# Kernel optimization log

Hardware: AMD Instinct MI355X
Metric: run time of the kernel (lower is better)

## Reference

```python
import jax, jax.numpy as jnp
import numpy as np

N0, N1, N2 = 500000, 100000, 20000
E1, E2 = 1600000, 320000
DIN, DH, DOUT = 128, 256, 128
EPS_BN = 1e-5
EPS_NORM = 1e-12


def setup_inputs() -> dict:
    key = jax.random.key(0)
    k = jax.random.split(key, 16)
    s = 0.05
    return {
        "x": jax.random.normal(k[0], (N0, DIN), jnp.float32),
        "src1": jax.random.randint(k[1], (E1,), 0, N0),
        "dst1": jax.random.randint(k[2], (E1,), 0, N1),
        "src2": jax.random.randint(k[3], (E2,), 0, N1),
        "dst2": jax.random.randint(k[4], (E2,), 0, N2),
        "n1": N1,
        "n2": N2,
        "W1_1": jax.random.normal(k[5], (DH, DIN), jnp.float32) * s,
        "W2_1": jax.random.normal(k[6], (DH, DIN), jnp.float32) * s,
        "b2_1": jax.random.normal(k[7], (DH,), jnp.float32) * s,
        "gamma1": jax.random.uniform(k[8], (DH,), jnp.float32, 0.5, 1.5),
        "beta1": jax.random.normal(k[9], (DH,), jnp.float32) * s,
        "mean1": jax.random.normal(k[10], (DH,), jnp.float32) * s,
        "var1": jax.random.uniform(k[11], (DH,), jnp.float32, 0.5, 1.5),
        "W1_2": jax.random.normal(k[12], (DOUT, DH), jnp.float32) * s,
        "W2_2": jax.random.normal(k[13], (DOUT, DH), jnp.float32) * s,
        "b2_2": jax.random.normal(k[14], (DOUT,), jnp.float32) * s,
    }


def _mean_agg(h, src, dst, n_target):
    # torch_sparse.matmul(adj_t, h, reduce='mean'): per-target mean of neighbor rows
    ssum = jax.ops.segment_sum(h[src], dst, num_segments=n_target)
    cnt = jax.ops.segment_sum(jnp.ones(src.shape, h.dtype), dst, num_segments=n_target)
    return ssum / jnp.maximum(cnt, 1.0)[:, None]


def _l2norm(h):
    # F.normalize(h, p=2, dim=1)
    n = jnp.sqrt(jnp.sum(h * h, axis=1, keepdims=True))
    return h / jnp.maximum(n, EPS_NORM)


def reference(x, src1, dst1, src2, dst2, n1, n2,
              W1_1, W2_1, b2_1, gamma1, beta1, mean1, var1,
              W1_2, W2_2, b2_2):
    # --- layer 1: SageConv(in=128, out=256) ---
    h_n = _mean_agg(x, src1, dst1, n1)                 # [n1, DIN]
    h = x[:n1] @ W1_1.T + (h_n @ W2_1.T + b2_1)        # [n1, DH]
    h = _l2norm(h)
    # BatchNorm1d (eval mode: running stats), then ReLU; dropout is identity in eval
    h = gamma1 * (h - mean1) * jax.lax.rsqrt(var1 + EPS_BN) + beta1
    h = jax.nn.relu(h)
    # --- layer 2: SageConv(in=256, out=128) ---
    h_n2 = _mean_agg(h, src2, dst2, n2)                # [n2, DH]
    out = h[:n2] @ W1_2.T + (h_n2 @ W2_2.T + b2_2)     # [n2, DOUT]
    return _l2norm(out)
```

## Files before the change

### kernel.cpp

```cpp
#include <hip/hip_runtime.h>
#include <hip/hip_bf16.h>

#define N1C  100000
#define N2C  20000
#define DIN_ 128
#define DH_  256
#define DOUT_ 128
#define CAP_LOG2 6
#define CAP_     64

#define BIN_SHIFT 7
#define NBIN1 782
#define NBIN2 157
#define NBINS 939
#define CAP_BIN 3072
#define CHUNK_A 8192

typedef unsigned short ushort_t;
typedef unsigned int   uint_t;
typedef __attribute__((ext_vector_type(8))) short bf16x8;
typedef __attribute__((ext_vector_type(4))) float f32x4;

__device__ __forceinline__ float bf2f(ushort_t u) {
    return __uint_as_float(((uint_t)u) << 16);
}
__device__ __forceinline__ ushort_t f2bf(float f) {
    uint_t x = __float_as_uint(f);
    x += 0x7fffu + ((x >> 16) & 1u);
    return (ushort_t)(x >> 16);
}

__global__ __launch_bounds__(256) void convert_all_kernel(
    const float* __restrict__ src, ushort_t* __restrict__ dst, long long n8,
    const float* __restrict__ w0, const float* __restrict__ w1,
    const float* __restrict__ w2, const float* __restrict__ w3,
    ushort_t* __restrict__ wdst)
{
    const long long t = (long long)blockIdx.x * 256 + threadIdx.x;
    if (t < n8) {
        const float4 v0 = *(const float4*)(src + t * 8);
        const float4 v1 = *(const float4*)(src + t * 8 + 4);
        uint4 o;
        o.x = (uint_t)f2bf(v0.x) | ((uint_t)f2bf(v0.y) << 16);
        o.y = (uint_t)f2bf(v0.z) | ((uint_t)f2bf(v0.w) << 16);
        o.z = (uint_t)f2bf(v1.x) | ((uint_t)f2bf(v1.y) << 16);
        o.w = (uint_t)f2bf(v1.z) | ((uint_t)f2bf(v1.w) << 16);
        *(uint4*)(dst + t * 8) = o;
    } else {
        const long long t2 = t - n8;
        if (t2 >= 16384) return;
        const int mat = (int)(t2 >> 12);
        const long long idx = (long long)(t2 & 4095) * 8;
        const float* s = (mat == 0) ? w0 : (mat == 1) ? w1 : (mat == 2) ? w2 : w3;
        const float4 v0 = *(const float4*)(s + idx);
        const float4 v1 = *(const float4*)(s + idx + 4);
        uint4 o;
        o.x = (uint_t)f2bf(v0.x) | ((uint_t)f2bf(v0.y) << 16);
        o.y = (uint_t)f2bf(v0.z) | ((uint_t)f2bf(v0.w) << 16);
        o.z = (uint_t)f2bf(v1.x) | ((uint_t)f2bf(v1.y) << 16);
        o.w = (uint_t)f2bf(v1.z) | ((uint_t)f2bf(v1.w) << 16);
        *(uint4*)(wdst + (long long)mat * 32768 + idx) = o;
    }
}

__global__ __launch_bounds__(256) void bin_edges_kernel(
    const int* __restrict__ src1, const int* __restrict__ dst1, int E1,
    const int* __restrict__ src2, const int* __restrict__ dst2, int E2,
    int* __restrict__ gTail, uint2* __restrict__ binBuf)
{
    __shared__ int hist[NBINS];
    __shared__ int binOff[NBINS];
    __shared__ int runc[NBINS];
    __shared__ int gb[NBINS];
    __shared__ uint2 stage[CHUNK_A];
    __shared__ int wtot[4];

    const int tid = threadIdx.x;
    const int tE = E1 + E2;
    const int c0 = blockIdx.x * CHUNK_A;
    const int cend = (c0 + CHUNK_A < tE) ? (c0 + CHUNK_A) : tE;
    const int ccnt = cend - c0;

    for (int b = tid; b < NBINS; b += 256) hist[b] = 0;
    __syncthreads();

    for (int i = c0 + tid; i < cend; i += 256) {
        int d, bin;
        if (i < E1) { d = dst1[i];      bin = d >> BIN_SHIFT; }
        else        { d = dst2[i - E1]; bin = NBIN1 + (d >> BIN_SHIFT); }
        atomicAdd(&hist[bin], 1);
    }
    __syncthreads();

    {
        int h[4]; int tsum = 0;
        #pragma unroll
        for (int k = 0; k < 4; ++k) {
            const int b = tid * 4 + k;
            h[k] = (b < NBINS) ? hist[b] : 0;
            tsum += h[k];
        }
        int s = tsum;
        #pragma unroll
        for (int o = 1; o < 64; o <<= 1) {
            int t = __shfl_up(s, (unsigned)o);
            if ((tid & 63) >= o) s += t;
        }
        if ((tid & 63) == 63) wtot[tid >> 6] = s;
        __syncthreads();
        int wpre = 0;
        #pragma unroll
        for (int k = 0; k < 4; ++k) wpre += (k < (tid >> 6)) ? wtot[k] : 0;
        int run = wpre + (s - tsum);
        #pragma unroll
        for (int k = 0; k < 4; ++k) {
            const int b = tid * 4 + k;
            if (b < NBINS) {
                binOff[b] = run;
                runc[b]   = run;
                gb[b] = h[k] ? atomicAdd(&gTail[b], h[k]) : 0;
            }
            run += h[k];
        }
    }
    __syncthreads();

    for (int i = c0 + tid; i < cend; i += 256) {
        int s, d, bin;
        if (i < E1) { s = src1[i];      d = dst1[i];      bin = d >> BIN_SHIFT; }
        else        { s = src2[i - E1]; d = dst2[i - E1]; bin = NBIN1 + (d >> BIN_SHIFT); }
        const int r = atomicAdd(&runc[bin], 1);
        stage[r] = make_uint2((uint_t)s, (uint_t)d | ((uint_t)bin << 17));
    }
    __syncthreads();

    for (int i = tid; i < ccnt; i += 256) {
        const uint2 u = stage[i];
        const int bin = (int)(u.y >> 17);
        const int local = gb[bin] + (i - binOff[bin]);
        if (local < CAP_BIN)
            binBuf[(size_t)bin * CAP_BIN + local] = u;
    }
}

__global__ __launch_bounds__(256) void build_buckets_kernel(
    const int* __restrict__ gTail, const uint2* __restrict__ binBuf,
    int* __restrict__ cnt1, int* __restrict__ esrc1,
    int* __restrict__ cnt2, int* __restrict__ esrc2)
{
    __shared__ int run[128];
    __shared__ int eLDS[128 * CAP_];

    const int b = blockIdx.x;
    const int tid = threadIdx.x;
    const int t0 = gTail[b];
    const int nE = (t0 < CAP_BIN) ? t0 : CAP_BIN;
    const bool g2 = (b >= NBIN1);
    const int lb = g2 ? (b - NBIN1) : b;
    const int d0 = lb << BIN_SHIFT;
    const int n  = g2 ? N2C : N1C;
    int* cnt  = g2 ? cnt2  : cnt1;
    int* esrc = g2 ? esrc2 : esrc1;

    for (int k = tid; k < 128; k += 256) run[k] = 0;
    __syncthreads();

    const uint2* bp = binBuf + (size_t)b * CAP_BIN;
    for (int i = tid; i < nE; i += 256) {
        const uint2 u = bp[i];
        const int ld = (int)(u.y & 127u);
        const int slot = atomicAdd(&run[ld], 1);
        if (slot < CAP_) eLDS[(ld << CAP_LOG2) + slot] = (int)u.x;
    }
    __syncthreads();

    const int nd = ((n - d0) < 128) ? (n - d0) : 128;
    const int tot4 = (nd << CAP_LOG2) >> 2;
    int4* dstp = (int4*)(esrc + ((size_t)d0 << CAP_LOG2));
    const int4* srcp = (const int4*)eLDS;
    for (int i = tid; i < tot4; i += 256) dstp[i] = srcp[i];
    for (int k = tid; k < nd; k += 256) cnt[d0 + k] = run[k];
}

__global__ __launch_bounds__(256) void gather_mean_128_bf16(
    const ushort_t* __restrict__ X, const int* __restrict__ cnt,
    const int* __restrict__ esrc, ushort_t* __restrict__ agg, int n)
{
    const int w = (blockIdx.x * 256 + threadIdx.x) >> 6;
    const int lane = threadIdx.x & 63;
    if (w >= n) return;
    const int deg = cnt[w];
    const int end = (deg < CAP_) ? deg : CAP_;
    const int* ep = esrc + ((size_t)w << CAP_LOG2);
    const int c = lane << 1;
    float ax = 0.f, ay = 0.f;
    int e = 0;
    for (; e + 3 < end; e += 4) {
        const int s0 = ep[e], s1 = ep[e+1], s2 = ep[e+2], s3 = ep[e+3];
        const uint_t u0 = *(const uint_t*)(X + (size_t)s0 * DIN_ + c);
        const uint_t u1 = *(const uint_t*)(X + (size_t)s1 * DIN_ + c);
        const uint_t u2 = *(const uint_t*)(X + (size_t)s2 * DIN_ + c);
        const uint_t u3 = *(const uint_t*)(X + (size_t)s3 * DIN_ + c);
        ax += bf2f((ushort_t)u0) + bf2f((ushort_t)u1)
            + bf2f((ushort_t)u2) + bf2f((ushort_t)u3);
        ay += bf2f((ushort_t)(u0 >> 16)) + bf2f((ushort_t)(u1 >> 16))
            + bf2f((ushort_t)(u2 >> 16)) + bf2f((ushort_t)(u3 >> 16));
    }
    for (; e < end; ++e) {
        const uint_t u0 = *(const uint_t*)(X + (size_t)ep[e] * DIN_ + c);
        ax += bf2f((ushort_t)u0);
        ay += bf2f((ushort_t)(u0 >> 16));
    }
    const float r = 1.0f / fmaxf((float)deg, 1.0f);
    const uint_t o = (uint_t)f2bf(ax * r) | ((uint_t)f2bf(ay * r) << 16);
    *(uint_t*)(agg + (size_t)w * DIN_ + c) = o;
}

__global__ __launch_bounds__(256) void gather_mean_256_bf16(
    const ushort_t* __restrict__ X, const int* __restrict__ cnt,
    const int* __restrict__ esrc, ushort_t* __restrict__ agg, int n)
{
    const int w = (blockIdx.x * 256 + threadIdx.x) >> 6;
    const int lane = threadIdx.x & 63;
    if (w >= n) return;
    const int deg = cnt[w];
    const int end = (deg < CAP_) ? deg : CAP_;
    const int* ep = esrc + ((size_t)w << CAP_LOG2);
    const int c = lane << 2;
    float a0 = 0.f, a1 = 0.f, a2 = 0.f, a3 = 0.f;
    int e = 0;
    for (; e + 3 < end; e += 4) {
        const int s0 = ep[e], s1 = ep[e+1], s2 = ep[e+2], s3 = ep[e+3];
        const uint2 u0 = *(const uint2*)(X + (size_t)s0 * DH_ + c);
        const uint2 u1 = *(const uint2*)(X + (size_t)s1 * DH_ + c);
        const uint2 u2 = *(const uint2*)(X + (size_t)s2 * DH_ + c);
        const uint2 u3 = *(const uint2*)(X + (size_t)s3 * DH_ + c);
        a0 += bf2f((ushort_t)u0.x) + bf2f((ushort_t)u1.x)
            + bf2f((ushort_t)u2.x) + bf2f((ushort_t)u3.x);
        a1 += bf2f((ushort_t)(u0.x >> 16)) + bf2f((ushort_t)(u1.x >> 16))
            + bf2f((ushort_t)(u2.x >> 16)) + bf2f((ushort_t)(u3.x >> 16));
        a2 += bf2f((ushort_t)u0.y) + bf2f((ushort_t)u1.y)
            + bf2f((ushort_t)u2.y) + bf2f((ushort_t)u3.y);
        a3 += bf2f((ushort_t)(u0.y >> 16)) + bf2f((ushort_t)(u1.y >> 16))
            + bf2f((ushort_t)(u2.y >> 16)) + bf2f((ushort_t)(u3.y >> 16));
    }
    for (; e < end; ++e) {
        const uint2 u0 = *(const uint2*)(X + (size_t)ep[e] * DH_ + c);
        a0 += bf2f((ushort_t)u0.x);
        a1 += bf2f((ushort_t)(u0.x >> 16));
        a2 += bf2f((ushort_t)u0.y);
        a3 += bf2f((ushort_t)(u0.y >> 16));
    }
    const float r = 1.0f / fmaxf((float)deg, 1.0f);
    uint2 o;
    o.x = (uint_t)f2bf(a0 * r) | ((uint_t)f2bf(a1 * r) << 16);
    o.y = (uint_t)f2bf(a2 * r) | ((uint_t)f2bf(a3 * r) << 16);
    *(uint2*)(agg + (size_t)w * DH_ + c) = o;
}

__global__ __launch_bounds__(256) void gemm1_fused(
    const ushort_t* __restrict__ A1, const ushort_t* __restrict__ B1,
    const ushort_t* __restrict__ A2, const ushort_t* __restrict__ B2,
    const float* __restrict__ bias,
    const float* __restrict__ gamma, const float* __restrict__ beta,
    const float* __restrict__ mean, const float* __restrict__ var,
    ushort_t* __restrict__ H, int M)
{
    __shared__ ushort_t As[64][40];
    __shared__ ushort_t Bs[256][40];
    __shared__ float rowss[4][64];

    const int tid = threadIdx.x;
    const int m0 = blockIdx.x * 64;

    const int ar = tid >> 2;
    const int aq = (tid & 3) * 8;
    const bool arow_ok = (m0 + ar) < M;

    const int wid  = tid >> 6;
    const int lane = tid & 63;
    const int lm   = lane & 15;
    const int lqq  = lane >> 4;
    const int wcol = wid * 64;

    const f32x4 fzero = {0.f, 0.f, 0.f, 0.f};
    f32x4 acc[4][4];
    #pragma unroll
    for (int i = 0; i < 4; ++i)
        #pragma unroll
        for (int j = 0; j < 4; ++j) acc[i][j] = fzero;

    #pragma unroll
    for (int phase = 0; phase < 2; ++phase) {
        const ushort_t* __restrict__ A = phase ? A2 : A1;
        const ushort_t* __restrict__ B = phase ? B2 : B1;
        const ushort_t* Ap = A + (size_t)(m0 + ar) * 128 + aq;
        const ushort_t* Bp = B + (size_t)tid * 128;

        #pragma unroll
        for (int k0 = 0; k0 < 128; k0 += 32) {
            uint4 a = {0, 0, 0, 0};
            if (arow_ok) a = *(const uint4*)(Ap + k0);
            const uint4 b0 = *(const uint4*)(Bp + k0);
            const uint4 b1 = *(const uint4*)(Bp + k0 + 8);
            const uint4 b2 = *(const uint4*)(Bp + k0 + 16);
            const uint4 b3 = *(const uint4*)(Bp + k0 + 24);

            __syncthreads();
            *(uint4*)&As[ar][aq]   = a;
            *(uint4*)&Bs[tid][0]   = b0;
            *(uint4*)&Bs[tid][8]   = b1;
            *(uint4*)&Bs[tid][16]  = b2;
            *(uint4*)&Bs[tid][24]  = b3;
            __syncthreads();

            bf16x8 af[4], bfr[4];
            #pragma unroll
            for (int i = 0; i < 4; ++i)
                af[i] = *(const bf16x8*)&As[i * 16 + lm][lqq * 8];
            #pragma unroll
            for (int j = 0; j < 4; ++j)
                bfr[j] = *(const bf16x8*)&Bs[wcol + j * 16 + lm][lqq * 8];

            #pragma unroll
            for (int i = 0; i < 4; ++i)
                #pragma unroll
                for (int j = 0; j < 4; ++j)
                    acc[i][j] = __builtin_amdgcn_mfma_f32_16x16x32_bf16(
                        af[i], bfr[j], acc[i][j], 0, 0, 0);
        }
    }

    float bj[4], sc[4], sh[4];
    #pragma unroll
    for (int j = 0; j < 4; ++j) {
        const int C = wcol + j * 16 + lm;
        bj[j] = bias[C];
        const float is = rsqrtf(var[C] + 1e-5f);
        sc[j] = gamma[C] * is;
        sh[j] = beta[C] - mean[C] * gamma[C] * is;
    }

    float ss[4][4];
    #pragma unroll
    for (int i = 0; i < 4; ++i) {
        #pragma unroll
        for (int r = 0; r < 4; ++r) {
            float s = 0.f;
            #pragma unroll
            for (int j = 0; j < 4; ++j) {
                const float v = acc[i][j][r] + bj[j];
                acc[i][j][r] = v;
                s += v * v;
            }
            s += __shfl_xor(s, 1);
            s += __shfl_xor(s, 2);
            s += __shfl_xor(s, 4);
            s += __shfl_xor(s, 8);
            ss[i][r] = s;
        }
    }
    if (lm == 0) {
        #pragma unroll
        for (int i = 0; i < 4; ++i)
            #pragma unroll
            for (int r = 0; r < 4; ++r)
                rowss[wid][i * 16 + lqq * 4 + r] = ss[i][r];
    }
    __syncthreads();

    #pragma unroll
    for (int i = 0; i < 4; ++i) {
        #pragma unroll
        for (int r = 0; r < 4; ++r) {
            const int R = i * 16 + lqq * 4 + r;
            const float tot = rowss[0][R] + rowss[1][R] + rowss[2][R] + rowss[3][R];
            const float inv = 1.0f / fmaxf(sqrtf(tot), 1e-12f);
            const int row = m0 + R;
            if (row < M) {
                const size_t base = (size_t)row * DH_ + wcol + lm;
                #pragma unroll
                for (int j = 0; j < 4; ++j) {
                    const float v = fmaxf(acc[i][j][r] * inv * sc[j] + sh[j], 0.f);
                    H[base + j * 16] = f2bf(v);
                }
            }
        }
    }
}

__global__ __launch_bounds__(256) void gemm2_fused(
    const ushort_t* __restrict__ A1, const ushort_t* __restrict__ B1,
    const ushort_t* __restrict__ A2, const ushort_t* __restrict__ B2,
    const float* __restrict__ bias,
    float* __restrict__ Cout, int M)
{
    __shared__ ushort_t As[128][40];
    __shared__ ushort_t Bs[128][40];
    __shared__ float rowss[2][128];

    const int tid = threadIdx.x;
    const int m0 = blockIdx.x * 128;

    const int lr = tid >> 1;
    const int lq = (tid & 1) * 8;

    const int wid  = tid >> 6;
    const int lane = tid & 63;
    const int lm   = lane & 15;
    const int lqq  = lane >> 4;
    const int wrow = (wid >> 1) * 64;
    const int wcol = (wid & 1) * 64;
    const int wc   = wid & 1;

    const f32x4 fzero = {0.f, 0.f, 0.f, 0.f};
    f32x4 acc[4][4];
    #pragma unroll
    for (int i = 0; i < 4; ++i)
        #pragma unroll
        for (int j = 0; j < 4; ++j) acc[i][j] = fzero;

    const bool arow_ok = (m0 + lr) < M;

    #pragma unroll
    for (int phase = 0; phase < 2; ++phase) {
        const ushort_t* __restrict__ A = phase ? A2 : A1;
        const ushort_t* __restrict__ B = phase ? B2 : B1;
        const ushort_t* Ap = A + (size_t)(m0 + lr) * 256 + lq;
        const ushort_t* Bp = B + (size_t)lr * 256 + lq;

        for (int k0 = 0; k0 < 256; k0 += 32) {
            uint4 a0 = {0, 0, 0, 0}, a1 = {0, 0, 0, 0};
            if (arow_ok) {
                a0 = *(const uint4*)(Ap + k0);
                a1 = *(const uint4*)(Ap + k0 + 16);
            }
            const uint4 b0 = *(const uint4*)(Bp + k0);
            const uint4 b1 = *(const uint4*)(Bp + k0 + 16);

            __syncthreads();
            *(uint4*)&As[lr][lq]      = a0;
            *(uint4*)&As[lr][lq + 16] = a1;
            *(uint4*)&Bs[lr][lq]      = b0;
            *(uint4*)&Bs[lr][lq + 16] = b1;
            __syncthreads();

            bf16x8 af[4], bfr[4];
            #pragma unroll
            for (int i = 0; i < 4; ++i)
                af[i] = *(const bf16x8*)&As[wrow + i * 16 + lm][lqq * 8];
            #pragma unroll
            for (int j = 0; j < 4; ++j)
                bfr[j] = *(const bf16x8*)&Bs[wcol + j * 16 + lm][lqq * 8];

            #pragma unroll
            for (int i = 0; i < 4; ++i)
                #pragma unroll
                for (int j = 0; j < 4; ++j)
                    acc[i][j] = __builtin_amdgcn_mfma_f32_16x16x32_bf16(
                        af[i], bfr[j], acc[i][j], 0, 0, 0);
        }
    }

    float bj[4];
    #pragma unroll
    for (int j = 0; j < 4; ++j) bj[j] = bias[wcol + j * 16 + lm];

    float ss[4][4];
    #pragma unroll
    for (int i = 0; i < 4; ++i) {
        #pragma unroll
        for (int r = 0; r < 4; ++r) {
            float s = 0.f;
            #pragma unroll
            for (int j = 0; j < 4; ++j) {
                const float v = acc[i][j][r] + bj[j];
                acc[i][j][r] = v;
                s += v * v;
            }
            s += __shfl_xor(s, 1);
            s += __shfl_xor(s, 2);
            s += __shfl_xor(s, 4);
            s += __shfl_xor(s, 8);
            ss[i][r] = s;
        }
    }
    if (lm == 0) {
        #pragma unroll
        for (int i = 0; i < 4; ++i)
            #pragma unroll
            for (int r = 0; r < 4; ++r)
                rowss[wc][wrow + i * 16 + lqq * 4 + r] = ss[i][r];
    }
    __syncthreads();

    #pragma unroll
    for (int i = 0; i < 4; ++i) {
        #pragma unroll
        for (int r = 0; r < 4; ++r) {
            const int R = wrow + i * 16 + lqq * 4 + r;
            const float tot = rowss[0][R] + rowss[1][R];
            const float inv = 1.0f / fmaxf(sqrtf(tot), 1e-12f);
            const int row = m0 + R;
            if (row < M) {
                const size_t base = (size_t)row * DOUT_ + wcol + lm;
                #pragma unroll
                for (int j = 0; j < 4; ++j)
                    Cout[base + j * 16] = acc[i][j][r] * inv;
            }
        }
    }
}

extern "C" void kernel_launch(void* const* d_in, const int* in_sizes, int n_in,
                              void* d_out, int out_size, void* d_ws, size_t ws_size,
                              hipStream_t stream)
{
    const float* x     = (const float*)d_in[0];
    const int*   src1  = (const int*)d_in[1];
    const int*   dst1  = (const int*)d_in[2];
    const int*   src2  = (const int*)d_in[3];
    const int*   dst2  = (const int*)d_in[4];
    const float* W1_1  = (const float*)d_in[7];
    const float* W2_1  = (const float*)d_in[8];
    const float* b2_1  = (const float*)d_in[9];
    const float* gamma1= (const float*)d_in[10];
    const float* beta1 = (const float*)d_in[11];
    const float* mean1 = (const float*)d_in[12];
    const float* var1  = (const float*)d_in[13];
    const float* W1_2  = (const float*)d_in[14];
    const float* W2_2  = (const float*)d_in[15];
    const float* b2_2  = (const float*)d_in[16];
    float* out = (float*)d_out;

    const int E1 = in_sizes[1];
    const int E2 = in_sizes[3];
    const int n1 = N1C;
    const int n2 = N2C;

    char* wsb = (char*)d_ws;
    ushort_t* xb     = (ushort_t*)(wsb + 0);
    ushort_t* h      = (ushort_t*)(wsb + 128000000);
    ushort_t* agg1   = (ushort_t*)(wsb + 179200000);
    ushort_t* agg2   = (ushort_t*)(wsb + 204800000);
    int*      esrc1  = (int*)(wsb + 215040000);
    int*      esrc2  = (int*)(wsb + 240640000);
    int*      cnt1   = (int*)(wsb + 245760000);
    int*      cnt2   = (int*)(wsb + 246160000);
    ushort_t* wb     = (ushort_t*)(wsb + 246240000);
    int*      gTail  = (int*)(wsb + 246502400);
    uint2*    binBuf = (uint2*)(wsb + 246507520);
    ushort_t* w11b = wb;
    ushort_t* w21b = wb + 32768;
    ushort_t* w12b = wb + 65536;
    ushort_t* w22b = wb + 98304;

    {
        const long long n8 = (long long)500000 * DIN_ / 8;
        const int nblk = (int)(n8 / 256) + 64;
        convert_all_kernel<<<nblk, 256, 0, stream>>>(x, xb, n8,
                                                     W1_1, W2_1, W1_2, W2_2, wb);
    }

    hipMemsetAsync(gTail, 0, NBINS * sizeof(int), stream);
    {
        const int tE = E1 + E2;
        const int nblkA = (tE + CHUNK_A - 1) / CHUNK_A;
        bin_edges_kernel<<<nblkA, 256, 0, stream>>>(
            src1, dst1, E1, src2, dst2, E2, gTail, binBuf);
        build_buckets_kernel<<<NBINS, 256, 0, stream>>>(
            gTail, binBuf, cnt1, esrc1, cnt2, esrc2);
    }

    gather_mean_128_bf16<<<(n1 + 3) / 4, 256, 0, stream>>>(xb, cnt1, esrc1, agg1, n1);
    gemm1_fused<<<(n1 + 63) / 64, 256, 0, stream>>>(
        xb, w11b, agg1, w21b, b2_1, gamma1, beta1, mean1, var1, h, n1);

    gather_mean_256_bf16<<<(n2 + 3) / 4, 256, 0, stream>>>(h, cnt2, esrc2, agg2, n2);
    gemm2_fused<<<(n2 + 127) / 128, 256, 0, stream>>>(
        h, w12b, agg2, w22b, b2_2, out, n2);
}
```

Measured before the change: 651.1 us.

## Fuse bf16 conversion with edge binning and build buckets inside gather kernels

Merges the x/weight bf16 conversion into the edge-binning kernel as extra blocks, so the two independent phases share one launch and can overlap. Removes the separate build_buckets pass and its global esrc/cnt arrays: each gather block now reads its bin from binBuf, builds per-destination neighbour lists in LDS, and aggregates directly. The binning chunk size is halved. In exchange, each bin is scanned twice (once per 64-row half), and the gather blocks are larger and use more LDS, which may lower occupancy.

```diff
diff --git a/kernel.cpp b/kernel.cpp
--- a/kernel.cpp
+++ b/kernel.cpp
@@ -14,7 +14,7 @@
 #define NBIN2 157
 #define NBINS 939
 #define CAP_BIN 3072
-#define CHUNK_A 8192
+#define CHUNK_A 4096
 
 typedef unsigned short ushort_t;
 typedef unsigned int   uint_t;
@@ -30,43 +30,14 @@
     return (ushort_t)(x >> 16);
 }
 
-__global__ __launch_bounds__(256) void convert_all_kernel(
-    const float* __restrict__ src, ushort_t* __restrict__ dst, long long n8,
+__global__ __launch_bounds__(256) void convert_and_bin_kernel(
+    const float* __restrict__ xsrc, ushort_t* __restrict__ xdst, long long n8,
     const float* __restrict__ w0, const float* __restrict__ w1,
     const float* __restrict__ w2, const float* __restrict__ w3,
-    ushort_t* __restrict__ wdst)
-{
-    const long long t = (long long)blockIdx.x * 256 + threadIdx.x;
-    if (t < n8) {
-        const float4 v0 = *(const float4*)(src + t * 8);
-        const float4 v1 = *(const float4*)(src + t * 8 + 4);
-        uint4 o;
-        o.x = (uint_t)f2bf(v0.x) | ((uint_t)f2bf(v0.y) << 16);
-        o.y = (uint_t)f2bf(v0.z) | ((uint_t)f2bf(v0.w) << 16);
-        o.z = (uint_t)f2bf(v1.x) | ((uint_t)f2bf(v1.y) << 16);
-        o.w = (uint_t)f2bf(v1.z) | ((uint_t)f2bf(v1.w) << 16);
-        *(uint4*)(dst + t * 8) = o;
-    } else {
-        const long long t2 = t - n8;
-        if (t2 >= 16384) return;
-        const int mat = (int)(t2 >> 12);
-        const long long idx = (long long)(t2 & 4095) * 8;
-        const float* s = (mat == 0) ? w0 : (mat == 1) ? w1 : (mat == 2) ? w2 : w3;
-        const float4 v0 = *(const float4*)(s + idx);
-        const float4 v1 = *(const float4*)(s + idx + 4);
-        uint4 o;
-        o.x = (uint_t)f2bf(v0.x) | ((uint_t)f2bf(v0.y) << 16);
-        o.y = (uint_t)f2bf(v0.z) | ((uint_t)f2bf(v0.w) << 16);
-        o.z = (uint_t)f2bf(v1.x) | ((uint_t)f2bf(v1.y) << 16);
-        o.w = (uint_t)f2bf(v1.z) | ((uint_t)f2bf(v1.w) << 16);
-        *(uint4*)(wdst + (long long)mat * 32768 + idx) = o;
-    }
-}
-
-__global__ __launch_bounds__(256) void bin_edges_kernel(
+    ushort_t* __restrict__ wdst,
     const int* __restrict__ src1, const int* __restrict__ dst1, int E1,
     const int* __restrict__ src2, const int* __restrict__ dst2, int E2,
-    int* __restrict__ gTail, uint2* __restrict__ binBuf)
+    int* __restrict__ gTail, uint2* __restrict__ binBuf, int nbA)
 {
     __shared__ int hist[NBINS];
     __shared__ int binOff[NBINS];
@@ -76,6 +47,36 @@
     __shared__ int wtot[4];
 
     const int tid = threadIdx.x;
+
+    if ((int)blockIdx.x >= nbA) {
+        const long long t = (long long)((int)blockIdx.x - nbA) * 256 + tid;
+        if (t < n8) {
+            const float4 v0 = *(const float4*)(xsrc + t * 8);
+            const float4 v1 = *(const float4*)(xsrc + t * 8 + 4);
+            uint4 o;
+            o.x = (uint_t)f2bf(v0.x) | ((uint_t)f2bf(v0.y) << 16);
+            o.y = (uint_t)f2bf(v0.z) | ((uint_t)f2bf(v0.w) << 16);
+            o.z = (uint_t)f2bf(v1.x) | ((uint_t)f2bf(v1.y) << 16);
+            o.w = (uint_t)f2bf(v1.z) | ((uint_t)f2bf(v1.w) << 16);
+            *(uint4*)(xdst + t * 8) = o;
+        } else {
+            const long long t2 = t - n8;
+            if (t2 >= 16384) return;
+            const int mat = (int)(t2 >> 12);
+            const long long idx = (long long)(t2 & 4095) * 8;
+            const float* s = (mat == 0) ? w0 : (mat == 1) ? w1 : (mat == 2) ? w2 : w3;
+            const float4 v0 = *(const float4*)(s + idx);
+            const float4 v1 = *(const float4*)(s + idx + 4);
+            uint4 o;
+            o.x = (uint_t)f2bf(v0.x) | ((uint_t)f2bf(v0.y) << 16);
+            o.y = (uint_t)f2bf(v0.z) | ((uint_t)f2bf(v0.w) << 16);
+            o.z = (uint_t)f2bf(v1.x) | ((uint_t)f2bf(v1.y) << 16);
+            o.w = (uint_t)f2bf(v1.z) | ((uint_t)f2bf(v1.w) << 16);
+            *(uint4*)(wdst + (long long)mat * 32768 + idx) = o;
+        }
+        return;
+    }
+
     const int tE = E1 + E2;
     const int c0 = blockIdx.x * CHUNK_A;
     const int cend = (c0 + CHUNK_A < tE) ? (c0 + CHUNK_A) : tE;
@@ -143,119 +144,138 @@
     }
 }
 
-__global__ __launch_bounds__(256) void build_buckets_kernel(
-    const int* __restrict__ gTail, const uint2* __restrict__ binBuf,
-    int* __restrict__ cnt1, int* __restrict__ esrc1,
-    int* __restrict__ cnt2, int* __restrict__ esrc2)
+__global__ __launch_bounds__(512) void gather1_bucket_kernel(
+    const ushort_t* __restrict__ X, const int* __restrict__ gTail,
+    const uint2* __restrict__ binBuf, ushort_t* __restrict__ agg)
 {
-    __shared__ int run[128];
-    __shared__ int eLDS[128 * CAP_];
-
-    const int b = blockIdx.x;
+    __shared__ int run[64];
+    __shared__ int eLDS[64 * CAP_];
+
     const int tid = threadIdx.x;
-    const int t0 = gTail[b];
+    const int g0 = blockIdx.x << 6;
+    const int bin = g0 >> BIN_SHIFT;
+    const int half = (g0 >> 6) & 1;
+    const int t0 = gTail[bin];
     const int nE = (t0 < CAP_BIN) ? t0 : CAP_BIN;
-    const bool g2 = (b >= NBIN1);
-    const int lb = g2 ? (b - NBIN1) : b;
-    const int d0 = lb << BIN_SHIFT;
-    const int n  = g2 ? N2C : N1C;
-    int* cnt  = g2 ? cnt2  : cnt1;
-    int* esrc = g2 ? esrc2 : esrc1;
-
-    for (int k = tid; k < 128; k += 256) run[k] = 0;
-    __syncthreads();
-
-    const uint2* bp = binBuf + (size_t)b * CAP_BIN;
-    for (int i = tid; i < nE; i += 256) {
+
+    if (tid < 64) run[tid] = 0;
+    __syncthreads();
+
+    const uint2* bp = binBuf + (size_t)bin * CAP_BIN;
+    for (int i = tid; i < nE; i += 512) {
         const uint2 u = bp[i];
         const int ld = (int)(u.y & 127u);
-        const int slot = atomicAdd(&run[ld], 1);
-        if (slot < CAP_) eLDS[(ld << CAP_LOG2) + slot] = (int)u.x;
-    }
-    __syncthreads();
-
-    const int nd = ((n - d0) < 128) ? (n - d0) : 128;
-    const int tot4 = (nd << CAP_LOG2) >> 2;
-    int4* dstp = (int4*)(esrc + ((size_t)d0 << CAP_LOG2));
-    const int4* srcp = (const int4*)eLDS;
-    for (int i = tid; i < tot4; i += 256) dstp[i] = srcp[i];
-    for (int k = tid; k < nd; k += 256) cnt[d0 + k] = run[k];
-}
-
-__global__ __launch_bounds__(256) void gather_mean_128_bf16(
-    const ushort_t* __restrict__ X, const int* __restrict__ cnt,
-    const int* __restrict__ esrc, ushort_t* __restrict__ agg, int n)
+        if ((ld >> 6) == half) {
+            const int l = ld & 63;
+            const int slot = atomicAdd(&run[l], 1);
+            if (slot < CAP_) eLDS[(l << CAP_LOG2) + slot] = (int)u.x;
+        }
+    }
+    __syncthreads();
+
+    const int wid = tid >> 6, lane = tid & 63;
+    const int c = lane << 1;
+    #pragma unroll
+    for (int rr = 0; rr < 8; ++rr) {
+        const int l = (wid << 3) + rr;
+        const int d = g0 + l;
+        if (d >= N1C) break;
+        const int deg = run[l];
+        const int end = (deg < CAP_) ? deg : CAP_;
+        const int* ep = &eLDS[l << CAP_LOG2];
+        float ax = 0.f, ay = 0.f;
+        int e = 0;
+        for (; e + 3 < end; e += 4) {
+            const int s0 = ep[e], s1 = ep[e+1], s2 = ep[e+2], s3 = ep[e+3];
+            const uint_t u0 = *(const uint_t*)(X + (size_t)s0 * DIN_ + c);
+            const uint_t u1 = *(const uint_t*)(X + (size_t)s1 * DIN_ + c);
+            const uint_t u2 = *(const uint_t*)(X + (size_t)s2 * DIN_ + c);
+            const uint_t u3 = *(const uint_t*)(X + (size_t)s3 * DIN_ + c);
+            ax += bf2f((ushort_t)u0) + bf2f((ushort_t)u1)
+                + bf2f((ushort_t)u2) + bf2f((ushort_t)u3);
+            ay += bf2f((ushort_t)(u0 >> 16)) + bf2f((ushort_t)(u1 >> 16))
+                + bf2f((ushort_t)(u2 >> 16)) + bf2f((ushort_t)(u3 >> 16));
+        }
+        for (; e < end; ++e) {
+            const uint_t u0 = *(const uint_t*)(X + (size_t)ep[e] * DIN_ + c);
+            ax += bf2f((ushort_t)u0);
+            ay += bf2f((ushort_t)(u0 >> 16));
+        }
+        const float r = 1.0f / fmaxf((float)deg, 1.0f);
+        const uint_t o = (uint_t)f2bf(ax * r) | ((uint_t)f2bf(ay * r) << 16);
+        *(uint_t*)(agg + (size_t)d * DIN_ + c) = o;
+    }
+}
+
+__global__ __launch_bounds__(512) void gather2_bucket_kernel(
+    const ushort_t* __restrict__ X, const int* __restrict__ gTail,
+    const uint2* __restrict__ binBuf, ushort_t* __restrict__ agg)
 {
-    const int w = (blockIdx.x * 256 + threadIdx.x) >> 6;
-    const int lane = threadIdx.x & 63;
-    if (w >= n) return;
-    const int deg = cnt[w];
-    const int end = (deg < CAP_) ? deg : CAP_;
-    const int* ep = esrc + ((size_t)w << CAP_LOG2);
-    const int c = lane << 1;
-    float ax = 0.f, ay = 0.f;
-    int e = 0;
-    for (; e + 3 < end; e += 4) {
-        const int s0 = ep[e], s1 = ep[e+1], s2 = ep[e+2], s3 = ep[e+3];
-        const uint_t u0 = *(const uint_t*)(X + (size_t)s0 * DIN_ + c);
-        const uint_t u1 = *(const uint_t*)(X + (size_t)s1 * DIN_ + c);
-        const uint_t u2 = *(const uint_t*)(X + (size_t)s2 * DIN_ + c);
-        const uint_t u3 = *(const uint_t*)(X + (size_t)s3 * DIN_ + c);
-        ax += bf2f((ushort_t)u0) + bf2f((ushort_t)u1)
-            + bf2f((ushort_t)u2) + bf2f((ushort_t)u3);
-        ay += bf2f((ushort_t)(u0 >> 16)) + bf2f((ushort_t)(u1 >> 16))
-            + bf2f((ushort_t)(u2 >> 16)) + bf2f((ushort_t)(u3 >> 16));
-    }
-    for (; e < end; ++e) {
-        const uint_t u0 = *(const uint_t*)(X + (size_t)ep[e] * DIN_ + c);
-        ax += bf2f((ushort_t)u0);
-        ay += bf2f((ushort_t)(u0 >> 16));
-    }
-    const float r = 1.0f / fmaxf((float)deg, 1.0f);
-    const uint_t o = (uint_t)f2bf(ax * r) | ((uint_t)f2bf(ay * r) << 16);
-    *(uint_t*)(agg + (size_t)w * DIN_ + c) = o;
-}
-
-__global__ __launch_bounds__(256) void gather_mean_256_bf16(
-    const ushort_t* __restrict__ X, const int* __restrict__ cnt,
-    const int* __restrict__ esrc, ushort_t* __restrict__ agg, int n)
-{
-    const int w = (blockIdx.x * 256 + threadIdx.x) >> 6;
-    const int lane = threadIdx.x & 63;
-    if (w >= n) return;
-    const int deg = cnt[w];
-    const int end = (deg < CAP_) ? deg : CAP_;
-    const int* ep = esrc + ((size_t)w << CAP_LOG2);
+    __shared__ int run[64];
+    __shared__ int eLDS[64 * CAP_];
+
+    const int tid = threadIdx.x;
+    const int g0 = blockIdx.x << 6;
+    const int bin = NBIN1 + (g0 >> BIN_SHIFT);
+    const int half = (g0 >> 6) & 1;
+    const int t0 = gTail[bin];
+    const int nE = (t0 < CAP_BIN) ? t0 : CAP_BIN;
+
+    if (tid < 64) run[tid] = 0;
+    __syncthreads();
+
+    const uint2* bp = binBuf + (size_t)bin * CAP_BIN;
+    for (int i = tid; i < nE; i += 512) {
+        const uint2 u = bp[i];
+        const int ld = (int)(u.y & 127u);
+        if ((ld >> 6) == half) {
+            const int l = ld & 63;
+            const int slot = atomicAdd(&run[l], 1);
+            if (slot < CAP_) eLDS[(l << CAP_LOG2) + slot] = (int)u.x;
+        }
+    }
+    __syncthreads();
+
+    const int wid = tid >> 6, lane = tid & 63;
     const int c = lane << 2;
-    float a0 = 0.f, a1 = 0.f, a2 = 0.f, a3 = 0.f;
-    int e = 0;
-    for (; e + 3 < end; e += 4) {
-        const int s0 = ep[e], s1 = ep[e+1], s2 = ep[e+2], s3 = ep[e+3];
-        const uint2 u0 = *(const uint2*)(X + (size_t)s0 * DH_ + c);
-        const uint2 u1 = *(const uint2*)(X + (size_t)s1 * DH_ + c);
-        const uint2 u2 = *(const uint2*)(X + (size_t)s2 * DH_ + c);
-        const uint2 u3 = *(const uint2*)(X + (size_t)s3 * DH_ + c);
-        a0 += bf2f((ushort_t)u0.x) + bf2f((ushort_t)u1.x)
-            + bf2f((ushort_t)u2.x) + bf2f((ushort_t)u3.x);
-        a1 += bf2f((ushort_t)(u0.x >> 16)) + bf2f((ushort_t)(u1.x >> 16))
-            + bf2f((ushort_t)(u2.x >> 16)) + bf2f((ushort_t)(u3.x >> 16));
-        a2 += bf2f((ushort_t)u0.y) + bf2f((ushort_t)u1.y)
-            + bf2f((ushort_t)u2.y) + bf2f((ushort_t)u3.y);
-        a3 += bf2f((ushort_t)(u0.y >> 16)) + bf2f((ushort_t)(u1.y >> 16))
-            + bf2f((ushort_t)(u2.y >> 16)) + bf2f((ushort_t)(u3.y >> 16));
-    }
-    for (; e < end; ++e) {
-        const uint2 u0 = *(const uint2*)(X + (size_t)ep[e] * DH_ + c);
-        a0 += bf2f((ushort_t)u0.x);
-        a1 += bf2f((ushort_t)(u0.x >> 16));
-        a2 += bf2f((ushort_t)u0.y);
-        a3 += bf2f((ushort_t)(u0.y >> 16));
-    }
-    const float r = 1.0f / fmaxf((float)deg, 1.0f);
-    uint2 o;
-    o.x = (uint_t)f2bf(a0 * r) | ((uint_t)f2bf(a1 * r) << 16);
-    o.y = (uint_t)f2bf(a2 * r) | ((uint_t)f2bf(a3 * r) << 16);
-    *(uint2*)(agg + (size_t)w * DH_ + c) = o;
+    #pragma unroll
+    for (int rr = 0; rr < 8; ++rr) {
+        const int l = (wid << 3) + rr;
+        const int d = g0 + l;
+        if (d >= N2C) break;
+        const int deg = run[l];
+        const int end = (deg < CAP_) ? deg : CAP_;
+        const int* ep = &eLDS[l << CAP_LOG2];
+        float a0 = 0.f, a1 = 0.f, a2 = 0.f, a3 = 0.f;
+        int e = 0;
+        for (; e + 3 < end; e += 4) {
+            const int s0 = ep[e], s1 = ep[e+1], s2 = ep[e+2], s3 = ep[e+3];
+            const uint2 u0 = *(const uint2*)(X + (size_t)s0 * DH_ + c);
+            const uint2 u1 = *(const uint2*)(X + (size_t)s1 * DH_ + c);
+            const uint2 u2 = *(const uint2*)(X + (size_t)s2 * DH_ + c);
+            const uint2 u3 = *(const uint2*)(X + (size_t)s3 * DH_ + c);
+            a0 += bf2f((ushort_t)u0.x) + bf2f((ushort_t)u1.x)
+                + bf2f((ushort_t)u2.x) + bf2f((ushort_t)u3.x);
+            a1 += bf2f((ushort_t)(u0.x >> 16)) + bf2f((ushort_t)(u1.x >> 16))
+                + bf2f((ushort_t)(u2.x >> 16)) + bf2f((ushort_t)(u3.x >> 16));
+            a2 += bf2f((ushort_t)u0.y) + bf2f((ushort_t)u1.y)
+                + bf2f((ushort_t)u2.y) + bf2f((ushort_t)u3.y);
+            a3 += bf2f((ushort_t)(u0.y >> 16)) + bf2f((ushort_t)(u1.y >> 16))
+                + bf2f((ushort_t)(u2.y >> 16)) + bf2f((ushort_t)(u3.y >> 16));
+        }
+        for (; e < end; ++e) {
+            const uint2 u0 = *(const uint2*)(X + (size_t)ep[e] * DH_ + c);
+            a0 += bf2f((ushort_t)u0.x);
+            a1 += bf2f((ushort_t)(u0.x >> 16));
+            a2 += bf2f((ushort_t)u0.y);
+            a3 += bf2f((ushort_t)(u0.y >> 16));
+        }
+        const float r = 1.0f / fmaxf((float)deg, 1.0f);
+        uint2 o;
+        o.x = (uint_t)f2bf(a0 * r) | ((uint_t)f2bf(a1 * r) << 16);
+        o.y = (uint_t)f2bf(a2 * r) | ((uint_t)f2bf(a3 * r) << 16);
+        *(uint2*)(agg + (size_t)d * DH_ + c) = o;
+    }
 }
 
 __global__ __launch_bounds__(256) void gemm1_fused(
@@ -543,40 +563,30 @@
     ushort_t* h      = (ushort_t*)(wsb + 128000000);
     ushort_t* agg1   = (ushort_t*)(wsb + 179200000);
     ushort_t* agg2   = (ushort_t*)(wsb + 204800000);
-    int*      esrc1  = (int*)(wsb + 215040000);
-    int*      esrc2  = (int*)(wsb + 240640000);
-    int*      cnt1   = (int*)(wsb + 245760000);
-    int*      cnt2   = (int*)(wsb + 246160000);
-    ushort_t* wb     = (ushort_t*)(wsb + 246240000);
-    int*      gTail  = (int*)(wsb + 246502400);
-    uint2*    binBuf = (uint2*)(wsb + 246507520);
+    ushort_t* wb     = (ushort_t*)(wsb + 215040000);
+    int*      gTail  = (int*)(wsb + 215302144);
+    uint2*    binBuf = (uint2*)(wsb + 215306240);
     ushort_t* w11b = wb;
     ushort_t* w21b = wb + 32768;
     ushort_t* w12b = wb + 65536;
     ushort_t* w22b = wb + 98304;
 
+    hipMemsetAsync(gTail, 0, NBINS * sizeof(int), stream);
     {
         const long long n8 = (long long)500000 * DIN_ / 8;
-        const int nblk = (int)(n8 / 256) + 64;
-        convert_all_kernel<<<nblk, 256, 0, stream>>>(x, xb, n8,
-                                                     W1_1, W2_1, W1_2, W2_2, wb);
-    }
-
-    hipMemsetAsync(gTail, 0, NBINS * sizeof(int), stream);
-    {
         const int tE = E1 + E2;
-        const int nblkA = (tE + CHUNK_A - 1) / CHUNK_A;
-        bin_edges_kernel<<<nblkA, 256, 0, stream>>>(
-            src1, dst1, E1, src2, dst2, E2, gTail, binBuf);
-        build_buckets_kernel<<<NBINS, 256, 0, stream>>>(
-            gTail, binBuf, cnt1, esrc1, cnt2, esrc2);
-    }
-
-    gather_mean_128_bf16<<<(n1 + 3) / 4, 256, 0, stream>>>(xb, cnt1, esrc1, agg1, n1);
+        const int nbA = (tE + CHUNK_A - 1) / CHUNK_A;
+        const int nblk = nbA + (int)(n8 / 256) + 64;
+        convert_and_bin_kernel<<<nblk, 256, 0, stream>>>(
+            x, xb, n8, W1_1, W2_1, W1_2, W2_2, wb,
+            src1, dst1, E1, src2, dst2, E2, gTail, binBuf, nbA);
+    }
+
+    gather1_bucket_kernel<<<(n1 + 63) / 64, 512, 0, stream>>>(xb, gTail, binBuf, agg1);
     gemm1_fused<<<(n1 + 63) / 64, 256, 0, stream>>>(
         xb, w11b, agg1, w21b, b2_1, gamma1, beta1, mean1, var1, h, n1);
 
-    gather_mean_256_bf16<<<(n2 + 3) / 4, 256, 0, stream>>>(h, cnt2, esrc2, agg2, n2);
+    gather2_bucket_kernel<<<(n2 + 63) / 64, 512, 0, stream>>>(h, gTail, binBuf, agg2);
     gemm2_fused<<<(n2 + 127) / 128, 256, 0, stream>>>(
         h, w12b, agg2, w22b, b2_2, out, n2);
 }
```

New measurement: 604.2 us. -7.2%, faster.
